# Kernel optimization log

Measured on AMD Instinct MI355X. Metric: run time of the kernel, lower is better.

Reference implementation:

```python
import jax, jax.numpy as jnp
import numpy as np

N = 100000
E = 800000
D_IN = 128
D_OUT = 128


def setup_inputs() -> dict:
    key = jax.random.key(0)
    k1, k2, k3, k4, k5 = jax.random.split(key, 5)
    x = jax.random.normal(k1, (N, D_IN), dtype=jnp.float32)
    edge_index = jax.random.randint(k2, (2, E), 0, N, dtype=jnp.int64)
    # xavier-uniform linear weight [out, in]
    lim_w = float(np.sqrt(6.0 / (D_IN + D_OUT)))
    lin_w = jax.random.uniform(k3, (D_OUT, D_IN), minval=-lim_w, maxval=lim_w, dtype=jnp.float32)
    # torch default bias init: U(-1/sqrt(fan_in), 1/sqrt(fan_in))
    lim_b = float(1.0 / np.sqrt(D_IN))
    lin_b = jax.random.uniform(k4, (D_OUT,), minval=-lim_b, maxval=lim_b, dtype=jnp.float32)
    lim_s = float(np.sqrt(6.0 / (D_OUT + D_OUT)))
    weight = jax.random.uniform(k5, (D_OUT, D_OUT), minval=-lim_s, maxval=lim_s, dtype=jnp.float32)
    return {"x": x, "edge_index": edge_index, "lin_w": lin_w, "lin_b": lin_b, "weight": weight}


def reference(x, edge_index, lin_w, lin_b, weight):
    row, col = edge_index[0], edge_index[1]
    # mean aggregation: scatter-add gathered neighbor features, normalize by degree
    agg = jax.ops.segment_sum(x[col], row, num_segments=x.shape[0])  # [N, d_in]
    deg = jax.ops.segment_sum(jnp.ones_like(row, dtype=x.dtype), row, num_segments=x.shape[0])
    deg = jnp.maximum(deg, 1.0)
    out = agg / deg[:, None]
    out = out @ lin_w.T + lin_b          # linear
    out = out @ weight                    # trailing matmul
    return out
```

## Files before the change

kernel.cpp:

```cpp
#include <hip/hip_runtime.h>

#define N_NODES 100000
#define N_EDGES 800000
#define D 128
#define MAXDEG 40
#define YSTRIDE 132
#define HIST_B 896
#define HIST_T (HIST_B * 256)
#define PRE_Z 1563

typedef unsigned int u32;
typedef unsigned short u16;
typedef __attribute__((ext_vector_type(8))) short bf16x8;
typedef __attribute__((ext_vector_type(4))) float f32x4;

static __device__ __forceinline__ short f2bf(float f) {
    u32 u = __float_as_uint(f);
    u += 0x7FFFu + ((u >> 16) & 1u);
    return (short)(u >> 16);
}
static __device__ __forceinline__ u32 pack2(float lo, float hi) {
    return (u32)(u16)f2bf(lo) | ((u32)(u16)f2bf(hi) << 16);
}
static __device__ __forceinline__ float bf_lo(u32 u) { return __uint_as_float(u << 16); }
static __device__ __forceinline__ float bf_hi(u32 u) { return __uint_as_float(u & 0xFFFF0000u); }

__global__ __launch_bounds__(256) void pre_kernel(
    const float* __restrict__ lin_w, const float* __restrict__ lin_b,
    const float* __restrict__ weight,
    u32* __restrict__ deg16, u16* __restrict__ Mfrag, float* __restrict__ b2)
{
    int t = threadIdx.x;
    int blk = blockIdx.x;
    if (blk < PRE_Z) {
        int base = blk * 1024 + t * 4;
        #pragma unroll
        for (int k = 0; k < 4; ++k)
            if (base + k < N_NODES * 16) deg16[base + k] = 0u;
    } else if (blk < PRE_Z + 64) {
        int kk = (blk - PRE_Z) * 2 + (t >> 7);
        int n = t & 127;
        float acc = 0.f;
        for (int o = 0; o < D; ++o)
            acc += lin_w[o * D + kk] * weight[o * D + n];
        int idx = ((((n >> 4) * 4 + (kk >> 5)) * 64) + ((kk >> 3) & 3) * 16 + (n & 15)) * 8 + (kk & 7);
        Mfrag[idx] = (u16)f2bf(acc);
    } else if (blk == PRE_Z + 64 && t < D) {
        float acc = 0.f;
        for (int o = 0; o < D; ++o)
            acc += lin_b[o] * weight[o * D + t];
        b2[t] = acc;
    }
}

__global__ __launch_bounds__(256) void hist_kernel(
    const int* __restrict__ ei,
    u32* __restrict__ deg16, int* __restrict__ csr)
{
    int t = threadIdx.x;
    int blk = blockIdx.x;
    int e0 = blk * 256 + t;
    int e1 = e0 + HIST_T;
    int e2 = e0 + 2 * HIST_T;
    int e3 = e0 + 3 * HIST_T;
    int r0 = ei[e0];
    int r1 = ei[e1];
    int r2 = ei[e2];
    bool has3 = (e3 < N_EDGES);
    int r3 = has3 ? ei[e3] : 0;
    int c0 = ei[N_EDGES + e0];
    int c1 = ei[N_EDGES + e1];
    int c2 = ei[N_EDGES + e2];
    int c3 = has3 ? ei[N_EDGES + e3] : 0;
    u32 p0 = atomicAdd(deg16 + r0 * 16, 1u);
    u32 p1 = atomicAdd(deg16 + r1 * 16, 1u);
    u32 p2 = atomicAdd(deg16 + r2 * 16, 1u);
    u32 p3 = has3 ? atomicAdd(deg16 + r3 * 16, 1u) : (u32)MAXDEG;
    if (p0 < (u32)MAXDEG) csr[r0 * MAXDEG + (int)p0] = c0;
    if (p1 < (u32)MAXDEG) csr[r1 * MAXDEG + (int)p1] = c1;
    if (p2 < (u32)MAXDEG) csr[r2 * MAXDEG + (int)p2] = c2;
    if (p3 < (u32)MAXDEG) csr[r3 * MAXDEG + (int)p3] = c3;
}

__global__ __launch_bounds__(256) void transform_kernel(
    const float* __restrict__ x, const u16* __restrict__ Mfrag, u16* __restrict__ y)
{
    __shared__ float shX[32 * 128];
    __shared__ float shY[32 * YSTRIDE];
    int t = threadIdx.x;
    int blk = blockIdx.x;
    int wave = t >> 6, lane = t & 63;

    {
        const char* xb = (const char*)x + (size_t)blk * 32 * 512;
        char* shXb = (char*)shX;
        #pragma unroll
        for (int i = 0; i < 4; ++i) {
            int s = (i * 256 + t) * 16;
            int r = s >> 9;
            int cb = s & 511;
            int g = (r << 9) + (cb ^ ((r & 7) << 4));
            __builtin_amdgcn_global_load_lds(
                (const u32*)(xb + g),
                (u32*)(shXb + (i * 4096 + wave * 1024)),
                16, 0, 0);
        }
    }

    int rt = wave & 1, ch = wave >> 1;
    int quad = lane >> 4, mrow = lane & 15;
    int r = rt * 16 + mrow;
    int sw = (mrow & 7) << 4;

    const bf16x8* mb = (const bf16x8*)(Mfrag) + (ch * 4) * 4 * 64 + lane;

    asm volatile("s_waitcnt vmcnt(0)" ::: "memory");
    __syncthreads();

    f32x4 acc0 = {0.f, 0.f, 0.f, 0.f};
    f32x4 acc1 = {0.f, 0.f, 0.f, 0.f};
    f32x4 acc2 = {0.f, 0.f, 0.f, 0.f};
    f32x4 acc3 = {0.f, 0.f, 0.f, 0.f};

    const char* shXb = (const char*)shX;
    #pragma unroll
    for (int ks = 0; ks < 4; ++ks) {
        int base = quad * 32 + ks * 128;
        float4 lo = *(const float4*)(shXb + (r << 9) + (base ^ sw));
        float4 hi = *(const float4*)(shXb + (r << 9) + ((base + 16) ^ sw));
        bf16x8 a;
        a[0] = f2bf(lo.x); a[1] = f2bf(lo.y); a[2] = f2bf(lo.z); a[3] = f2bf(lo.w);
        a[4] = f2bf(hi.x); a[5] = f2bf(hi.y); a[6] = f2bf(hi.z); a[7] = f2bf(hi.w);

        bf16x8 b0 = mb[ks * 64 + 0 * 256];
        bf16x8 b1 = mb[ks * 64 + 1 * 256];
        bf16x8 b2f = mb[ks * 64 + 2 * 256];
        bf16x8 b3 = mb[ks * 64 + 3 * 256];
        acc0 = __builtin_amdgcn_mfma_f32_16x16x32_bf16(a, b0, acc0, 0, 0, 0);
        acc1 = __builtin_amdgcn_mfma_f32_16x16x32_bf16(a, b1, acc1, 0, 0, 0);
        acc2 = __builtin_amdgcn_mfma_f32_16x16x32_bf16(a, b2f, acc2, 0, 0, 0);
        acc3 = __builtin_amdgcn_mfma_f32_16x16x32_bf16(a, b3, acc3, 0, 0, 0);
    }

    {
        float* dst = shY + (size_t)(rt * 16 + quad * 4) * YSTRIDE + ch * 64 + mrow;
        #pragma unroll
        for (int rr = 0; rr < 4; ++rr) {
            dst[rr * YSTRIDE + 0 * 16] = acc0[rr];
            dst[rr * YSTRIDE + 1 * 16] = acc1[rr];
            dst[rr * YSTRIDE + 2 * 16] = acc2[rr];
            dst[rr * YSTRIDE + 3 * 16] = acc3[rr];
        }
    }
    __syncthreads();

    {
        int orow = t >> 3, seg = t & 7;
        const float* src = shY + (size_t)orow * YSTRIDE + seg * 16;
        u32 p[8];
        #pragma unroll
        for (int i = 0; i < 8; ++i)
            p[i] = pack2(src[2 * i], src[2 * i + 1]);
        u32* dst = (u32*)y + ((size_t)(blk * 32 + orow) * 64 + seg * 8);
        *(uint4*)(dst + 0) = make_uint4(p[0], p[1], p[2], p[3]);
        *(uint4*)(dst + 4) = make_uint4(p[4], p[5], p[6], p[7]);
    }
}

__global__ __launch_bounds__(256) void gather_kernel(
    const u16* __restrict__ y, const int* __restrict__ csr,
    const u32* __restrict__ deg16,
    const float* __restrict__ b2, float* __restrict__ out)
{
    int idx = blockIdx.x * 256 + threadIdx.x;
    int n = idx >> 4;
    int sl = idx & 15;
    if (n >= N_NODES) return;
    u32 dn = deg16[n * 16];
    u32 cnt = (dn > (u32)MAXDEG) ? (u32)MAXDEG : dn;
    const int* cp = csr + (size_t)n * MAXDEG;
    const u32* yw = (const u32*)y;
    float a0 = 0.f, a1 = 0.f, a2 = 0.f, a3 = 0.f;
    float a4 = 0.f, a5 = 0.f, a6 = 0.f, a7 = 0.f;
    u32 e = 0;
    for (; e + 4 <= cnt; e += 4) {
        int c0 = cp[e + 0];
        int c1 = cp[e + 1];
        int c2 = cp[e + 2];
        int c3 = cp[e + 3];
        uint4 u0 = *(const uint4*)(yw + (size_t)c0 * 64 + sl * 4);
        uint4 u1 = *(const uint4*)(yw + (size_t)c1 * 64 + sl * 4);
        uint4 u2 = *(const uint4*)(yw + (size_t)c2 * 64 + sl * 4);
        uint4 u3 = *(const uint4*)(yw + (size_t)c3 * 64 + sl * 4);
        a0 += (bf_lo(u0.x) + bf_lo(u1.x)) + (bf_lo(u2.x) + bf_lo(u3.x));
        a1 += (bf_hi(u0.x) + bf_hi(u1.x)) + (bf_hi(u2.x) + bf_hi(u3.x));
        a2 += (bf_lo(u0.y) + bf_lo(u1.y)) + (bf_lo(u2.y) + bf_lo(u3.y));
        a3 += (bf_hi(u0.y) + bf_hi(u1.y)) + (bf_hi(u2.y) + bf_hi(u3.y));
        a4 += (bf_lo(u0.z) + bf_lo(u1.z)) + (bf_lo(u2.z) + bf_lo(u3.z));
        a5 += (bf_hi(u0.z) + bf_hi(u1.z)) + (bf_hi(u2.z) + bf_hi(u3.z));
        a6 += (bf_lo(u0.w) + bf_lo(u1.w)) + (bf_lo(u2.w) + bf_lo(u3.w));
        a7 += (bf_hi(u0.w) + bf_hi(u1.w)) + (bf_hi(u2.w) + bf_hi(u3.w));
    }
    for (; e < cnt; ++e) {
        uint4 u0 = *(const uint4*)(yw + (size_t)cp[e] * 64 + sl * 4);
        a0 += bf_lo(u0.x); a1 += bf_hi(u0.x);
        a2 += bf_lo(u0.y); a3 += bf_hi(u0.y);
        a4 += bf_lo(u0.z); a5 += bf_hi(u0.z);
        a6 += bf_lo(u0.w); a7 += bf_hi(u0.w);
    }
    float inv = 1.0f / (float)((dn < 1u) ? 1u : dn);
    float4 bA = *(const float4*)(b2 + sl * 8);
    float4 bB = *(const float4*)(b2 + sl * 8 + 4);
    float4 oA, oB;
    oA.x = a0 * inv + bA.x;
    oA.y = a1 * inv + bA.y;
    oA.z = a2 * inv + bA.z;
    oA.w = a3 * inv + bA.w;
    oB.x = a4 * inv + bB.x;
    oB.y = a5 * inv + bB.y;
    oB.z = a6 * inv + bB.z;
    oB.w = a7 * inv + bB.w;
    float* op = out + (size_t)n * D + sl * 8;
    *(float4*)(op + 0) = oA;
    *(float4*)(op + 4) = oB;
}

extern "C" void kernel_launch(void* const* d_in, const int* in_sizes, int n_in,
                              void* d_out, int out_size, void* d_ws, size_t ws_size,
                              hipStream_t stream) {
    const float* x      = (const float*)d_in[0];
    const int*   ei     = (const int*)d_in[1];
    const float* lin_w  = (const float*)d_in[2];
    const float* lin_b  = (const float*)d_in[3];
    const float* weight = (const float*)d_in[4];
    float* out = (float*)d_out;

    char* ws = (char*)d_ws;
    const size_t YB2  = (size_t)N_NODES * D * sizeof(u16);
    const size_t DB   = (size_t)N_NODES * 16 * sizeof(u32);
    u16*   y     = (u16*)ws;
    u32*   deg16 = (u32*)(ws + YB2);
    u16*   Mfrag = (u16*)(ws + YB2 + DB);
    float* b2    = (float*)(ws + YB2 + DB + 32768);
    int*   csr   = (int*)(ws + YB2 + DB + 32768 + 512);

    pre_kernel<<<PRE_Z + 65, 256, 0, stream>>>(lin_w, lin_b, weight, deg16, Mfrag, b2);
    hist_kernel<<<HIST_B, 256, 0, stream>>>(ei, deg16, csr);
    transform_kernel<<<N_NODES / 32, 256, 0, stream>>>(x, Mfrag, y);
    gather_kernel<<<(N_NODES * 16 + 255) / 256, 256, 0, stream>>>(y, csr, deg16, b2, out);
}
```

Measured before the change: 198.4 us.

## Merge hist into pre kernel, memset degrees, two tiles per transform block, wider gather

Clears the degree array with hipMemsetAsync and folds the histogram/CSR build and the weight-fold precompute into a single kernel, removing one launch. The transform kernel now handles two 32-row tiles per block with both tiles' loads issued up front, so the second load overlaps the first tile's MFMA work. The gather loop is unrolled to eight neighbors and reads indices as int4 vectors to raise memory-level parallelism. These are several independent changes; the extra LDS per block in transform may reduce occupancy.

```diff
diff --git a/kernel.cpp b/kernel.cpp
--- a/kernel.cpp
+++ b/kernel.cpp
@@ -7,7 +7,8 @@
 #define YSTRIDE 132
 #define HIST_B 896
 #define HIST_T (HIST_B * 256)
-#define PRE_Z 1563
+#define TILES 3125
+#define TB2 1563
 
 typedef unsigned int u32;
 typedef unsigned short u16;
@@ -25,27 +26,46 @@
 static __device__ __forceinline__ float bf_lo(u32 u) { return __uint_as_float(u << 16); }
 static __device__ __forceinline__ float bf_hi(u32 u) { return __uint_as_float(u & 0xFFFF0000u); }
 
-__global__ __launch_bounds__(256) void pre_kernel(
+__global__ __launch_bounds__(256) void hist_pre_kernel(
+    const int* __restrict__ ei,
     const float* __restrict__ lin_w, const float* __restrict__ lin_b,
     const float* __restrict__ weight,
-    u32* __restrict__ deg16, u16* __restrict__ Mfrag, float* __restrict__ b2)
+    u32* __restrict__ deg16, int* __restrict__ csr,
+    u16* __restrict__ Mfrag, float* __restrict__ b2)
 {
     int t = threadIdx.x;
     int blk = blockIdx.x;
-    if (blk < PRE_Z) {
-        int base = blk * 1024 + t * 4;
-        #pragma unroll
-        for (int k = 0; k < 4; ++k)
-            if (base + k < N_NODES * 16) deg16[base + k] = 0u;
-    } else if (blk < PRE_Z + 64) {
-        int kk = (blk - PRE_Z) * 2 + (t >> 7);
+    if (blk < HIST_B) {
+        int e0 = blk * 256 + t;
+        int e1 = e0 + HIST_T;
+        int e2 = e0 + 2 * HIST_T;
+        int e3 = e0 + 3 * HIST_T;
+        int r0 = ei[e0];
+        int r1 = ei[e1];
+        int r2 = ei[e2];
+        bool has3 = (e3 < N_EDGES);
+        int r3 = has3 ? ei[e3] : 0;
+        int c0 = ei[N_EDGES + e0];
+        int c1 = ei[N_EDGES + e1];
+        int c2 = ei[N_EDGES + e2];
+        int c3 = has3 ? ei[N_EDGES + e3] : 0;
+        u32 p0 = atomicAdd(deg16 + r0 * 16, 1u);
+        u32 p1 = atomicAdd(deg16 + r1 * 16, 1u);
+        u32 p2 = atomicAdd(deg16 + r2 * 16, 1u);
+        u32 p3 = has3 ? atomicAdd(deg16 + r3 * 16, 1u) : (u32)MAXDEG;
+        if (p0 < (u32)MAXDEG) csr[r0 * MAXDEG + (int)p0] = c0;
+        if (p1 < (u32)MAXDEG) csr[r1 * MAXDEG + (int)p1] = c1;
+        if (p2 < (u32)MAXDEG) csr[r2 * MAXDEG + (int)p2] = c2;
+        if (p3 < (u32)MAXDEG) csr[r3 * MAXDEG + (int)p3] = c3;
+    } else if (blk < 960) {
+        int kk = (blk - HIST_B) * 2 + (t >> 7);
         int n = t & 127;
         float acc = 0.f;
         for (int o = 0; o < D; ++o)
             acc += lin_w[o * D + kk] * weight[o * D + n];
         int idx = ((((n >> 4) * 4 + (kk >> 5)) * 64) + ((kk >> 3) & 3) * 16 + (n & 15)) * 8 + (kk & 7);
         Mfrag[idx] = (u16)f2bf(acc);
-    } else if (blk == PRE_Z + 64 && t < D) {
+    } else if (blk == 960 && t < D) {
         float acc = 0.f;
         for (int o = 0; o < D; ++o)
             acc += lin_b[o] * weight[o * D + t];
@@ -53,81 +73,22 @@
     }
 }
 
-__global__ __launch_bounds__(256) void hist_kernel(
-    const int* __restrict__ ei,
-    u32* __restrict__ deg16, int* __restrict__ csr)
-{
-    int t = threadIdx.x;
-    int blk = blockIdx.x;
-    int e0 = blk * 256 + t;
-    int e1 = e0 + HIST_T;
-    int e2 = e0 + 2 * HIST_T;
-    int e3 = e0 + 3 * HIST_T;
-    int r0 = ei[e0];
-    int r1 = ei[e1];
-    int r2 = ei[e2];
-    bool has3 = (e3 < N_EDGES);
-    int r3 = has3 ? ei[e3] : 0;
-    int c0 = ei[N_EDGES + e0];
-    int c1 = ei[N_EDGES + e1];
-    int c2 = ei[N_EDGES + e2];
-    int c3 = has3 ? ei[N_EDGES + e3] : 0;
-    u32 p0 = atomicAdd(deg16 + r0 * 16, 1u);
-    u32 p1 = atomicAdd(deg16 + r1 * 16, 1u);
-    u32 p2 = atomicAdd(deg16 + r2 * 16, 1u);
-    u32 p3 = has3 ? atomicAdd(deg16 + r3 * 16, 1u) : (u32)MAXDEG;
-    if (p0 < (u32)MAXDEG) csr[r0 * MAXDEG + (int)p0] = c0;
-    if (p1 < (u32)MAXDEG) csr[r1 * MAXDEG + (int)p1] = c1;
-    if (p2 < (u32)MAXDEG) csr[r2 * MAXDEG + (int)p2] = c2;
-    if (p3 < (u32)MAXDEG) csr[r3 * MAXDEG + (int)p3] = c3;
-}
-
-__global__ __launch_bounds__(256) void transform_kernel(
-    const float* __restrict__ x, const u16* __restrict__ Mfrag, u16* __restrict__ y)
-{
-    __shared__ float shX[32 * 128];
-    __shared__ float shY[32 * YSTRIDE];
-    int t = threadIdx.x;
-    int blk = blockIdx.x;
-    int wave = t >> 6, lane = t & 63;
-
-    {
-        const char* xb = (const char*)x + (size_t)blk * 32 * 512;
-        char* shXb = (char*)shX;
-        #pragma unroll
-        for (int i = 0; i < 4; ++i) {
-            int s = (i * 256 + t) * 16;
-            int r = s >> 9;
-            int cb = s & 511;
-            int g = (r << 9) + (cb ^ ((r & 7) << 4));
-            __builtin_amdgcn_global_load_lds(
-                (const u32*)(xb + g),
-                (u32*)(shXb + (i * 4096 + wave * 1024)),
-                16, 0, 0);
-        }
-    }
-
-    int rt = wave & 1, ch = wave >> 1;
-    int quad = lane >> 4, mrow = lane & 15;
+static __device__ __forceinline__ void compute_tile(
+    const char* __restrict__ bufb, float* __restrict__ shY,
+    const bf16x8* __restrict__ mb, u16* __restrict__ y,
+    int tile, int t, int rt, int ch, int quad, int mrow, int sw)
+{
     int r = rt * 16 + mrow;
-    int sw = (mrow & 7) << 4;
-
-    const bf16x8* mb = (const bf16x8*)(Mfrag) + (ch * 4) * 4 * 64 + lane;
-
-    asm volatile("s_waitcnt vmcnt(0)" ::: "memory");
-    __syncthreads();
-
     f32x4 acc0 = {0.f, 0.f, 0.f, 0.f};
     f32x4 acc1 = {0.f, 0.f, 0.f, 0.f};
     f32x4 acc2 = {0.f, 0.f, 0.f, 0.f};
     f32x4 acc3 = {0.f, 0.f, 0.f, 0.f};
 
-    const char* shXb = (const char*)shX;
     #pragma unroll
     for (int ks = 0; ks < 4; ++ks) {
         int base = quad * 32 + ks * 128;
-        float4 lo = *(const float4*)(shXb + (r << 9) + (base ^ sw));
-        float4 hi = *(const float4*)(shXb + (r << 9) + ((base + 16) ^ sw));
+        float4 lo = *(const float4*)(bufb + (r << 9) + (base ^ sw));
+        float4 hi = *(const float4*)(bufb + (r << 9) + ((base + 16) ^ sw));
         bf16x8 a;
         a[0] = f2bf(lo.x); a[1] = f2bf(lo.y); a[2] = f2bf(lo.z); a[3] = f2bf(lo.w);
         a[4] = f2bf(hi.x); a[5] = f2bf(hi.y); a[6] = f2bf(hi.z); a[7] = f2bf(hi.w);
@@ -161,9 +122,66 @@
         #pragma unroll
         for (int i = 0; i < 8; ++i)
             p[i] = pack2(src[2 * i], src[2 * i + 1]);
-        u32* dst = (u32*)y + ((size_t)(blk * 32 + orow) * 64 + seg * 8);
+        u32* dst = (u32*)y + ((size_t)(tile * 32 + orow) * 64 + seg * 8);
         *(uint4*)(dst + 0) = make_uint4(p[0], p[1], p[2], p[3]);
         *(uint4*)(dst + 4) = make_uint4(p[4], p[5], p[6], p[7]);
+    }
+}
+
+__global__ __launch_bounds__(256) void transform_kernel(
+    const float* __restrict__ x, const u16* __restrict__ Mfrag, u16* __restrict__ y)
+{
+    __shared__ float shX[2 * 32 * 128];
+    __shared__ float shY[32 * YSTRIDE];
+    int t = threadIdx.x;
+    int blk = blockIdx.x;
+    int wave = t >> 6, lane = t & 63;
+    int rt = wave & 1, ch = wave >> 1;
+    int quad = lane >> 4, mrow = lane & 15;
+    int sw = (mrow & 7) << 4;
+
+    int tile0 = blk * 2;
+    int tile1 = blk * 2 + 1;
+    bool has1 = (tile1 < TILES);
+
+    {
+        char* shXb = (char*)shX;
+        #pragma unroll
+        for (int i = 0; i < 4; ++i) {
+            int s = (i * 256 + t) * 16;
+            int rr = s >> 9;
+            int cb = s & 511;
+            int g = (rr << 9) + (cb ^ ((rr & 7) << 4));
+            __builtin_amdgcn_global_load_lds(
+                (const u32*)((const char*)x + (size_t)tile0 * 16384 + g),
+                (u32*)(shXb + i * 4096 + wave * 1024), 16, 0, 0);
+        }
+        if (has1) {
+            #pragma unroll
+            for (int i = 0; i < 4; ++i) {
+                int s = (i * 256 + t) * 16;
+                int rr = s >> 9;
+                int cb = s & 511;
+                int g = (rr << 9) + (cb ^ ((rr & 7) << 4));
+                __builtin_amdgcn_global_load_lds(
+                    (const u32*)((const char*)x + (size_t)tile1 * 16384 + g),
+                    (u32*)(shXb + 16384 + i * 4096 + wave * 1024), 16, 0, 0);
+            }
+        }
+    }
+
+    const bf16x8* mb = (const bf16x8*)(Mfrag) + (ch * 4) * 4 * 64 + lane;
+
+    if (has1) asm volatile("s_waitcnt vmcnt(4)" ::: "memory");
+    else      asm volatile("s_waitcnt vmcnt(0)" ::: "memory");
+    __builtin_amdgcn_s_barrier();
+    __builtin_amdgcn_sched_barrier(0);
+
+    compute_tile((const char*)shX, shY, mb, y, tile0, t, rt, ch, quad, mrow, sw);
+
+    if (has1) {
+        __syncthreads();
+        compute_tile((const char*)shX + 16384, shY, mb, y, tile1, t, rt, ch, quad, mrow, sw);
     }
 }
 
@@ -183,15 +201,40 @@
     float a0 = 0.f, a1 = 0.f, a2 = 0.f, a3 = 0.f;
     float a4 = 0.f, a5 = 0.f, a6 = 0.f, a7 = 0.f;
     u32 e = 0;
+    for (; e + 8 <= cnt; e += 8) {
+        int4 ca = *(const int4*)(cp + e);
+        int4 cb = *(const int4*)(cp + e + 4);
+        uint4 u0 = *(const uint4*)(yw + (size_t)ca.x * 64 + sl * 4);
+        uint4 u1 = *(const uint4*)(yw + (size_t)ca.y * 64 + sl * 4);
+        uint4 u2 = *(const uint4*)(yw + (size_t)ca.z * 64 + sl * 4);
+        uint4 u3 = *(const uint4*)(yw + (size_t)ca.w * 64 + sl * 4);
+        uint4 u4 = *(const uint4*)(yw + (size_t)cb.x * 64 + sl * 4);
+        uint4 u5 = *(const uint4*)(yw + (size_t)cb.y * 64 + sl * 4);
+        uint4 u6 = *(const uint4*)(yw + (size_t)cb.z * 64 + sl * 4);
+        uint4 u7 = *(const uint4*)(yw + (size_t)cb.w * 64 + sl * 4);
+        a0 += ((bf_lo(u0.x) + bf_lo(u1.x)) + (bf_lo(u2.x) + bf_lo(u3.x)))
+            + ((bf_lo(u4.x) + bf_lo(u5.x)) + (bf_lo(u6.x) + bf_lo(u7.x)));
+        a1 += ((bf_hi(u0.x) + bf_hi(u1.x)) + (bf_hi(u2.x) + bf_hi(u3.x)))
+            + ((bf_hi(u4.x) + bf_hi(u5.x)) + (bf_hi(u6.x) + bf_hi(u7.x)));
+        a2 += ((bf_lo(u0.y) + bf_lo(u1.y)) + (bf_lo(u2.y) + bf_lo(u3.y)))
+            + ((bf_lo(u4.y) + bf_lo(u5.y)) + (bf_lo(u6.y) + bf_lo(u7.y)));
+        a3 += ((bf_hi(u0.y) + bf_hi(u1.y)) + (bf_hi(u2.y) + bf_hi(u3.y)))
+            + ((bf_hi(u4.y) + bf_hi(u5.y)) + (bf_hi(u6.y) + bf_hi(u7.y)));
+        a4 += ((bf_lo(u0.z) + bf_lo(u1.z)) + (bf_lo(u2.z) + bf_lo(u3.z)))
+            + ((bf_lo(u4.z) + bf_lo(u5.z)) + (bf_lo(u6.z) + bf_lo(u7.z)));
+        a5 += ((bf_hi(u0.z) + bf_hi(u1.z)) + (bf_hi(u2.z) + bf_hi(u3.z)))
+            + ((bf_hi(u4.z) + bf_hi(u5.z)) + (bf_hi(u6.z) + bf_hi(u7.z)));
+        a6 += ((bf_lo(u0.w) + bf_lo(u1.w)) + (bf_lo(u2.w) + bf_lo(u3.w)))
+            + ((bf_lo(u4.w) + bf_lo(u5.w)) + (bf_lo(u6.w) + bf_lo(u7.w)));
+        a7 += ((bf_hi(u0.w) + bf_hi(u1.w)) + (bf_hi(u2.w) + bf_hi(u3.w)))
+            + ((bf_hi(u4.w) + bf_hi(u5.w)) + (bf_hi(u6.w) + bf_hi(u7.w)));
+    }
     for (; e + 4 <= cnt; e += 4) {
-        int c0 = cp[e + 0];
-        int c1 = cp[e + 1];
-        int c2 = cp[e + 2];
-        int c3 = cp[e + 3];
-        uint4 u0 = *(const uint4*)(yw + (size_t)c0 * 64 + sl * 4);
-        uint4 u1 = *(const uint4*)(yw + (size_t)c1 * 64 + sl * 4);
-        uint4 u2 = *(const uint4*)(yw + (size_t)c2 * 64 + sl * 4);
-        uint4 u3 = *(const uint4*)(yw + (size_t)c3 * 64 + sl * 4);
+        int4 ca = *(const int4*)(cp + e);
+        uint4 u0 = *(const uint4*)(yw + (size_t)ca.x * 64 + sl * 4);
+        uint4 u1 = *(const uint4*)(yw + (size_t)ca.y * 64 + sl * 4);
+        uint4 u2 = *(const uint4*)(yw + (size_t)ca.z * 64 + sl * 4);
+        uint4 u3 = *(const uint4*)(yw + (size_t)ca.w * 64 + sl * 4);
         a0 += (bf_lo(u0.x) + bf_lo(u1.x)) + (bf_lo(u2.x) + bf_lo(u3.x));
         a1 += (bf_hi(u0.x) + bf_hi(u1.x)) + (bf_hi(u2.x) + bf_hi(u3.x));
         a2 += (bf_lo(u0.y) + bf_lo(u1.y)) + (bf_lo(u2.y) + bf_lo(u3.y));
@@ -236,16 +279,17 @@
     float* out = (float*)d_out;
 
     char* ws = (char*)d_ws;
-    const size_t YB2  = (size_t)N_NODES * D * sizeof(u16);
-    const size_t DB   = (size_t)N_NODES * 16 * sizeof(u32);
+    const size_t YB2 = (size_t)N_NODES * D * sizeof(u16);
+    const size_t DB  = (size_t)N_NODES * 16 * sizeof(u32);
     u16*   y     = (u16*)ws;
     u32*   deg16 = (u32*)(ws + YB2);
     u16*   Mfrag = (u16*)(ws + YB2 + DB);
     float* b2    = (float*)(ws + YB2 + DB + 32768);
     int*   csr   = (int*)(ws + YB2 + DB + 32768 + 512);
 
-    pre_kernel<<<PRE_Z + 65, 256, 0, stream>>>(lin_w, lin_b, weight, deg16, Mfrag, b2);
-    hist_kernel<<<HIST_B, 256, 0, stream>>>(ei, deg16, csr);
-    transform_kernel<<<N_NODES / 32, 256, 0, stream>>>(x, Mfrag, y);
+    hipMemsetAsync(deg16, 0, DB, stream);
+
+    hist_pre_kernel<<<961, 256, 0, stream>>>(ei, lin_w, lin_b, weight, deg16, csr, Mfrag, b2);
+    transform_kernel<<<TB2, 256, 0, stream>>>(x, Mfrag, y);
     gather_kernel<<<(N_NODES * 16 + 255) / 256, 256, 0, stream>>>(y, csr, deg16, b2, out);
 }
```

After: 202.4 us. No clear change (+2.0%).
